# Kernel optimization log

Measured on AMD Instinct MI355X. Metric: run time of the kernel, lower is better.

The kernel has to match this reference:

```python
import jax, jax.numpy as jnp
import numpy as np

N_EVENTS = 50000
TS_SIZE = 512
N_NEURONS = 256
LAMBDA_HOMEO = 0.25


def setup_inputs() -> dict:
    key = jax.random.key(0)
    k1, k2 = jax.random.split(key)
    # event time surfaces (nonnegative, like torch surfaces)
    all_ts = jax.random.uniform(k1, (N_EVENTS, TS_SIZE), dtype=jnp.float32)
    # synapses.weight ~ U[0,1), as in torch.nn.init.uniform_(a=0,b=1)
    W = jax.random.uniform(k2, (N_NEURONS, TS_SIZE), dtype=jnp.float32)
    cumhisto = jnp.ones((N_NEURONS,), dtype=jnp.float32)
    return {"all_ts": all_ts, "W": W, "cumhisto": cumhisto}


def reference(all_ts, W, cumhisto):
    """Training branch (learning_flag=True, homeo_flag=True) of hotslayer.forward.

    Sequential per-event: normalize ts, cosine-like scores beta, homeostatic gain
    picks the winner, winner row of W is pulled toward ts, histogram incremented.
    Returns (per-event winners [N_EVENTS], final W [N,TS], final cumhisto [N]).
    """
    n_neurons = W.shape[0]

    def step(carry, ts):
        W, ch = carry
        ts = ts / jnp.linalg.norm(ts)
        w_norm = jnp.linalg.norm(W, axis=1)          # [N]
        beta = (W @ ts) / w_norm                      # [N]
        gain = jnp.exp(LAMBDA_HOMEO * (1.0 - n_neurons * ch / ch.sum()))
        n_star = jnp.argmax(gain * beta)
        Ck = W[n_star]                                # [TS]
        alpha = 0.01 / (1.0 + ch[n_star] / 20000.0)
        W = W.at[n_star].set(Ck + alpha * beta[n_star] * (ts - Ck))
        ch = ch.at[n_star].add(1.0)
        return (W, ch), n_star

    (W_f, ch_f), winners = jax.lax.scan(step, (W, cumhisto), all_ts)
    return winners, W_f, ch_f
```

## Files before the change

kernel.cpp:

```cpp
#include <hip/hip_runtime.h>
#include <hip/hip_bf16.h>

#define N_EVENTS 50000
#define TS 512
#define NN 256
#define BATCH 512
#define SUB 64
#define LAMB 0.25f
#define NB 98

#define RLF(v, l) __int_as_float(__builtin_amdgcn_readlane(__float_as_int(v), (l)))
#define RLI(v, l) __builtin_amdgcn_readlane((v), (l))
#define FRCP(x) __builtin_amdgcn_rcpf(x)
#define FRSQ(x) __builtin_amdgcn_rsqf(x)
#define DPP_MAXF(x, ctrl)                                                            \
    { int _s = __builtin_amdgcn_update_dpp(__float_as_int(x), __float_as_int(x),     \
                                           (ctrl), 0xF, 0xF, false);                 \
      (x) = fmaxf((x), __int_as_float(_s)); }


__global__ __launch_bounds__(256)
void inv_kernel(const float* __restrict__ ts, float* __restrict__ inv)
{
    __shared__ double red[256];
    const int e = blockIdx.x;
    const int d = threadIdx.x;
    const float* row = ts + (size_t)e * TS;
    float x0 = row[d], x1 = row[d + 256];
    red[d] = (double)x0 * x0 + (double)x1 * x1;
    __syncthreads();
    for (int st = 128; st > 0; st >>= 1) {
        if (d < st) red[d] += red[d + st];
        __syncthreads();
    }
    if (d == 0) inv[e] = (float)(1.0 / sqrt(red[0]));
}

__global__ __launch_bounds__(256)
void init_kernel(const float* __restrict__ chin, float* __restrict__ ch,
                 float* Pn0, float* Pn1, float* phi0, float* phi1,
                 float* c0, float* c1, float* d0, float* d1,
                 int* w0, int* w1)
{
    int i = blockIdx.x * 256 + threadIdx.x;
    if (i < NN) { ch[i] = chin[i]; Pn0[i] = 1.f; Pn1[i] = 1.f; }
    if (i < BATCH) {
        phi0[i] = 0.f; phi1[i] = 0.f; c0[i] = 0.f; c1[i] = 0.f;
        d0[i] = 0.f; d1[i] = 0.f; w0[i] = 0; w1[i] = 0;
    }
}


__device__ void gram_tile(float* SH, const float* __restrict__ ts,
                          const float* __restrict__ inv,
                          int astart, int as, int bstart2, int bs2,
                          int be, int bf, float* __restrict__ outp, int transpose)
{
    float* At = SH;
    float* Bt = SH + 64 * 33;
    if (be * 64 >= as || bf * 64 >= bs2) return;
    const int tx = threadIdx.x & 15, ty = threadIdx.x >> 4;
    float acc[4][4] = {};
    for (int kt = 0; kt < TS; kt += 32) {
        for (int it = threadIdx.x; it < 64 * 32; it += 256) {
            int r = it >> 5, c = it & 31;
            int ra = be * 64 + r, rb = bf * 64 + r;
            At[r * 33 + c] = (ra < as) ? ts[(size_t)(astart + ra) * TS + kt + c] : 0.f;
            Bt[r * 33 + c] = (rb < bs2) ? ts[(size_t)(bstart2 + rb) * TS + kt + c] : 0.f;
        }
        __syncthreads();
#pragma unroll
        for (int kk = 0; kk < 32; ++kk) {
            float av[4], bv[4];
#pragma unroll
            for (int i = 0; i < 4; ++i) av[i] = At[(ty * 4 + i) * 33 + kk];
#pragma unroll
            for (int j = 0; j < 4; ++j) bv[j] = Bt[(tx * 4 + j) * 33 + kk];
#pragma unroll
            for (int i = 0; i < 4; ++i)
#pragma unroll
                for (int j = 0; j < 4; ++j)
                    acc[i][j] += av[i] * bv[j];
        }
        __syncthreads();
    }
#pragma unroll
    for (int i = 0; i < 4; ++i) {
        int e = be * 64 + ty * 4 + i;
        if (e >= as) continue;
        float ie = inv[astart + e];
#pragma unroll
        for (int j = 0; j < 4; ++j) {
            int f = bf * 64 + tx * 4 + j;
            if (f >= bs2) continue;
            float v = acc[i][j] * ie * inv[bstart2 + f];
            if (transpose) outp[(size_t)f * BATCH + e] = v;
            else           outp[(size_t)e * BATCH + f] = v;
        }
    }
}

__global__ __launch_bounds__(256)
void gram_kernel(const float* __restrict__ ts, const float* __restrict__ inv,
                 float* __restrict__ outp, int astart, int as, int bstart2, int bs2,
                 int upper, int transpose)
{
    __shared__ float SHg[64 * 33 * 2];
    if (upper && (int)blockIdx.y < (int)blockIdx.x) return;
    gram_tile(SHg, ts, inv, astart, as, bstart2, bs2, blockIdx.x, blockIdx.y,
              outp, transpose);
}


__device__ void neuron_body(float* shf, double* red,
    const float* __restrict__ ts, const float* __restrict__ inv,
    const float* __restrict__ Wsrc, float* __restrict__ wdst,
    const int* __restrict__ winPrev, const float* __restrict__ phiPrev,
    const float* __restrict__ PnPrev,
    float* __restrict__ wn2W, float* __restrict__ S2W,
    const float* __restrict__ chbuf, float* __restrict__ chout,
    int n, int bprev_start, int bs_prev, int bnext_start, int bs_next)
{
    int* winS = (int*)shf;
    float* phiS = shf + 512;
    float* WL = shf + 1024;
    const int d = threadIdx.x;
    for (int i = d; i < bs_prev; i += 256) { winS[i] = winPrev[i]; phiS[i] = phiPrev[i]; }
    __syncthreads();
    const float Pf = PnPrev[n];
    float w0 = Wsrc[n * TS + d];
    float w1 = Wsrc[n * TS + d + 256];
    double a0 = 0.0, a1 = 0.0;
    for (int e = 0; e < bs_prev; ++e) {
        if (winS[e] == n) {
            double coef = (double)phiS[e];
            float iv = inv[bprev_start + e];
            const float* tr = ts + (size_t)(bprev_start + e) * TS;
            a0 += coef * (double)(tr[d] * iv);
            a1 += coef * (double)(tr[d + 256] * iv);
        }
    }
    w0 = (float)((double)Pf * ((double)w0 + a0));
    w1 = (float)((double)Pf * ((double)w1 + a1));
    wdst[n * TS + d] = w0;
    wdst[n * TS + d + 256] = w1;
    WL[d] = w0; WL[d + 256] = w1;
    if (wn2W) {
        red[d] = (double)w0 * w0 + (double)w1 * w1;
        __syncthreads();
        for (int st = 128; st > 0; st >>= 1) {
            if (d < st) red[d] += red[d + st];
            __syncthreads();
        }
        if (d == 0) wn2W[n] = (float)red[0];
    } else {
        __syncthreads();
    }
    if (bs_next > 0) {
#pragma unroll
        for (int rep = 0; rep < 2; ++rep) {
            int f = d + rep * 256;
            if (f < bs_next) {
                double acc = 0.0;
                const float* tr = ts + (size_t)(bnext_start + f) * TS;
                for (int k = 0; k < TS; ++k) acc += (double)tr[k] * (double)WL[k];
                S2W[f * NN + n] = (float)(acc * (double)inv[bnext_start + f]);
            }
        }
    }
    if (chout && d == 0) chout[n] = chbuf[n];
}

__global__ __launch_bounds__(256)
void neuron_kernel(const float* __restrict__ ts, const float* __restrict__ inv,
    const float* __restrict__ Wsrc, float* __restrict__ wdst,
    const int* __restrict__ winPrev, const float* __restrict__ phiPrev,
    const float* __restrict__ PnPrev,
    float* __restrict__ wn2W, float* __restrict__ S2W,
    const float* __restrict__ chbuf, float* __restrict__ chout,
    int bprev_start, int bs_prev, int bnext_start, int bs_next)
{
    __shared__ float SHN[1536];
    __shared__ double redN[256];
    neuron_body(SHN, redN, ts, inv, Wsrc, wdst, winPrev, phiPrev, PnPrev,
                wn2W, S2W, chbuf, chout, blockIdx.x,
                bprev_start, bs_prev, bnext_start, bs_next);
}


__global__ __launch_bounds__(256)
void fix_kernel(const float* __restrict__ S2r, const float* __restrict__ GxTr,
    const int* __restrict__ winPrev, const float* __restrict__ phiPrev,
    const float* __restrict__ cPrev, const float* __restrict__ dPrev,
    const float* __restrict__ PnPrev, const float* __restrict__ wn2b,
    float* __restrict__ S0corr, float* __restrict__ wn2start,
    int bs, int b0flag)
{
    __shared__ int winS[512];
    __shared__ float phiP[512];
    __shared__ float gr[512];
    __shared__ float cS[512];
    __shared__ float dS[512];
    const int tid = threadIdx.x;
    const int f = blockIdx.x;
    for (int i = tid; i < 512; i += 256) {
        int w = winPrev[i];
        winS[i] = w;
        phiP[i] = b0flag ? 0.f : phiPrev[i] * PnPrev[w];
        cS[i] = cPrev[i];
        dS[i] = dPrev[i];
        gr[i] = (b0flag || f >= bs) ? 0.f : GxTr[(size_t)f * BATCH + i];
    }
    __syncthreads();
    if (f < bs) {
        int n = tid;
        float acc = PnPrev[n] * S2r[f * NN + n];
        if (!b0flag) {
            for (int e = 0; e < 512; ++e)
                if (winS[e] == n) acc += phiP[e] * gr[e];
        }
        S0corr[f * NN + n] = acc;
    }
    if (f == 0 && tid < 64) {
        const int lane = tid;
        float w2[4];
#pragma unroll
        for (int k = 0; k < 4; ++k) w2[k] = wn2b[k * 64 + lane];
        for (int e = 0; e < 512; ++e) {
            float c = cS[e];
            if (c != 0.f) {
                int w = winS[e];
                int owner = w & 63, kk = w >> 6;
                float omc = 1.f - c;
                float t2 = 2.f * c * omc * dS[e] + c * c;
#pragma unroll
                for (int k = 0; k < 4; ++k)
                    if (lane == owner && k == kk) w2[k] = omc * omc * w2[k] + t2;
            }
        }
#pragma unroll
        for (int k = 0; k < 4; ++k) wn2start[k * 64 + lane] = w2[k];
    }
}


__device__ void block0_body(float* SH,
    const float* __restrict__ S0corr, const float* __restrict__ GwR,
    const float* __restrict__ wn2start, float* __restrict__ chbuf,
    int* __restrict__ winCur, float* __restrict__ phiCur,
    float* __restrict__ cCur, float* __restrict__ dotCur, float* __restrict__ PnCur,
    float* __restrict__ winners_out, int bstart, int bs)
{
    float* ACC = SH;
    float* GS  = SH + 16384;
    float* GL  = SH + 20480;
    int*   winL = (int*)(SH + 24576);
    float* phiL = SH + 25088;
    float* cL   = SH + 25600;
    float* dL   = SH + 26112;
    const int tid = threadIdx.x, wid = tid >> 6, lane = tid & 63;

    const float KC = -(LAMB * 256.0f * 1.44269504f);
    float ch[4] = {0,0,0,0}, wn2v[4] = {1,1,1,1};
    float rn[4] = {1,1,1,1}, Pn[4] = {1,1,1,1}, al[4] = {0,0,0,0};
    float Ssum = 1.f, K2 = 0.f;
    if (wid == 0) {
#pragma unroll
        for (int k = 0; k < 4; ++k) {
            int n = k * 64 + lane;
            ch[k] = chbuf[n];
            wn2v[k] = wn2start[n];
            rn[k] = FRSQ(wn2v[k]);
            al[k] = 0.01f * FRCP(1.0f + ch[k] * (1.0f / 20000.0f));
        }
        float loc = ch[0] + ch[1] + ch[2] + ch[3];
#pragma unroll
        for (int off = 32; off > 0; off >>= 1) loc += __shfl_xor(loc, off, 64);
        Ssum = loc;
        K2 = KC * FRCP(Ssum);
    }

    const int nsub = (bs + SUB - 1) >> 6;
    for (int sub = 0; sub < nsub; ++sub) {
        const int s0 = sub << 6;
        const int cnt = min(SUB, bs - s0);
        __syncthreads();
        {
            const int n = tid;
            for (int f = 0; f < cnt; f += 8) {
                const float* src = S0corr + (size_t)(s0 + f) * NN + n;
                float v0 = src[0 * NN], v1 = src[1 * NN], v2 = src[2 * NN], v3 = src[3 * NN];
                float v4 = src[4 * NN], v5 = src[5 * NN], v6 = src[6 * NN], v7 = src[7 * NN];
                ACC[(f + 0) * NN + ((n + f + 0) & 255)] = v0;
                ACC[(f + 1) * NN + ((n + f + 1) & 255)] = v1;
                ACC[(f + 2) * NN + ((n + f + 2) & 255)] = v2;
                ACC[(f + 3) * NN + ((n + f + 3) & 255)] = v3;
                ACC[(f + 4) * NN + ((n + f + 4) & 255)] = v4;
                ACC[(f + 5) * NN + ((n + f + 5) & 255)] = v5;
                ACC[(f + 6) * NN + ((n + f + 6) & 255)] = v6;
                ACC[(f + 7) * NN + ((n + f + 7) & 255)] = v7;
            }
        }
        for (int it = tid; it < SUB * SUB; it += 256) {
            int t = it >> 6, f = it & 63;
            GS[it] = (t < cnt && f < cnt) ? GwR[(size_t)(s0 + t) * BATCH + s0 + f] : 0.f;
        }
        for (int base = 0; base < s0; base += 64) {
            {
                const int i0 = tid, i1 = tid + 256, i2 = tid + 512, i3 = tid + 768;
                for (int rep = 0; rep < 4096; rep += 1024) {
                    float g0 = GwR[(size_t)(base + ((i0 + rep) >> 6)) * BATCH + s0 + (i0 & 63)];
                    float g1 = GwR[(size_t)(base + ((i1 + rep) >> 6)) * BATCH + s0 + (i1 & 63)];
                    float g2 = GwR[(size_t)(base + ((i2 + rep) >> 6)) * BATCH + s0 + (i2 & 63)];
                    float g3 = GwR[(size_t)(base + ((i3 + rep) >> 6)) * BATCH + s0 + (i3 & 63)];
                    GL[i0 + rep] = g0; GL[i1 + rep] = g1;
                    GL[i2 + rep] = g2; GL[i3 + rep] = g3;
                }
            }
            int wreg = winL[base + lane];
            float preg = phiL[base + lane];
            __syncthreads();
            for (int j = 0; j < 64; ++j) {
                int wj = RLI(wreg, j);
                if ((wj & 3) == wid) {
                    float pj = RLF(preg, j);
                    if (lane < cnt)
                        ACC[lane * NN + ((wj + lane) & 255)] += pj * GL[j * 64 + lane];
                }
            }
            __syncthreads();
        }
        __syncthreads();

        if (wid == 0) {
            float acur[4];
#pragma unroll
            for (int k = 0; k < 4; ++k) acur[k] = ACC[(k * 64 + lane) & 255];

            for (int t = 0; t < cnt; ++t) {
                const bool havenext = (t + 1 < cnt);
                float anext[4] = {0.f, 0.f, 0.f, 0.f};
                if (havenext) {
                    const int r = t + 1;
#pragma unroll
                    for (int k = 0; k < 4; ++k)
                        anext[k] = ACC[r * NN + ((k * 64 + lane + r) & 255)];
                }
                const int forig = t + 1 + lane;
                const float gval = GS[t * SUB + (forig & 63)];

                float beta[4], key[4];
#pragma unroll
                for (int k = 0; k < 4; ++k) {
                    float dot = Pn[k] * acur[k];
                    beta[k] = dot * rn[k];
                    key[k] = beta[k] * exp2f(K2 * ch[k]);
                }
                float kmax = fmaxf(fmaxf(key[0], key[1]), fmaxf(key[2], key[3]));
                DPP_MAXF(kmax, 0x111); DPP_MAXF(kmax, 0x112); DPP_MAXF(kmax, 0x114);
                DPP_MAXF(kmax, 0x118); DPP_MAXF(kmax, 0x142); DPP_MAXF(kmax, 0x143);
                const float smax = RLF(kmax, 63);

                unsigned long long m0 = __ballot(key[0] == smax);
                unsigned long long m1 = __ballot(key[1] == smax);
                unsigned long long m2 = __ballot(key[2] == smax);
                unsigned long long m3 = __ballot(key[3] == smax);
                int ns = m0 ? (int)__builtin_ctzll(m0)
                       : m1 ? 64  + (int)__builtin_ctzll(m1)
                       : m2 ? 128 + (int)__builtin_ctzll(m2)
                            : 192 + (int)__builtin_ctzll(m3);
                ns = __builtin_amdgcn_readfirstlane(ns);
                const int owner = ns & 63, ks = ns >> 6;

                float bsel = (ks == 0) ? beta[0] : (ks == 1) ? beta[1] : (ks == 2) ? beta[2] : beta[3];
                float asel = (ks == 0) ? acur[0] : (ks == 1) ? acur[1] : (ks == 2) ? acur[2] : acur[3];
                float psel = (ks == 0) ? Pn[0]   : (ks == 1) ? Pn[1]   : (ks == 2) ? Pn[2]   : Pn[3];
                float lsel = (ks == 0) ? al[0]   : (ks == 1) ? al[1]   : (ks == 2) ? al[2]   : al[3];
                const float betas  = RLF(bsel, owner);
                const float alphas = RLF(lsel, owner);
                const float dots   = RLF(psel * asel, owner);
                const float pold   = RLF(psel, owner);

                const float c    = alphas * betas;
                const float omc  = 1.0f - c;
                const float pnew = pold * omc;
                const float phi  = c * FRCP(pnew);
                const float g1   = RLF(gval, 0);

#pragma unroll
                for (int k = 0; k < 4; ++k) {
                    if (lane == owner && k == ks) {
                        wn2v[k] = omc * omc * wn2v[k] + 2.f * c * omc * dots + c * c;
                        rn[k] = FRSQ(wn2v[k]);
                        ch[k] += 1.0f;
                        al[k] = 0.01f * FRCP(1.0f + ch[k] * (1.0f / 20000.0f));
                        Pn[k] = pnew;
                        anext[k] += phi * g1;
                    }
                }
                if (lane > 0 && forig < cnt)
                    ACC[forig * NN + ((ns + forig) & 255)] += phi * gval;

                const int ib = s0 + t;
                if (lane == 0) {
                    winL[ib] = ns; phiL[ib] = phi;
                    cL[ib] = c; dL[ib] = dots;
                }
                Ssum += 1.0f;
                K2 = KC * FRCP(Ssum);
                if (havenext) {
#pragma unroll
                    for (int k = 0; k < 4; ++k) acur[k] = anext[k];
                }
            }
        }
    }
    __syncthreads();
    if (wid == 0) {
#pragma unroll
        for (int k = 0; k < 4; ++k) {
            int n = k * 64 + lane;
            chbuf[n] = ch[k];
            PnCur[n] = Pn[k];
        }
    }
    for (int i = tid; i < bs; i += 256) {
        int w = winL[i];
        winCur[i] = w;
        phiCur[i] = phiL[i];
        cCur[i] = cL[i];
        dotCur[i] = dL[i];
        winners_out[bstart + i] = (float)w;
    }
}


__global__ __launch_bounds__(256)
void fusedA_kernel(const float* __restrict__ ts, const float* __restrict__ inv,
    const float* __restrict__ S0corr, const float* __restrict__ GwR,
    float* __restrict__ GwW, float* __restrict__ GxTW,
    const float* __restrict__ wn2start, float* __restrict__ chbuf,
    const int* __restrict__ winPrev, const float* __restrict__ phiPrev,
    const float* __restrict__ PnPrev,
    int* __restrict__ winCur, float* __restrict__ phiCur,
    float* __restrict__ cCur, float* __restrict__ dotCur, float* __restrict__ PnCur,
    float* __restrict__ Wcur, float* __restrict__ wn2W, float* __restrict__ S2W,
    float* __restrict__ out, int b, int bstart, int bs, int bnext_start, int bs_next)
{
    __shared__ float SH[26624];
    const int bx = blockIdx.x;
    if (bx == 0) {
        block0_body(SH, S0corr, GwR, wn2start, chbuf,
                    winCur, phiCur, cCur, dotCur, PnCur, out, bstart, bs);
    } else if (bx <= NN) {
        neuron_body(SH, (double*)(SH + 1536), ts, inv, Wcur, Wcur,
                    winPrev, phiPrev, PnPrev, wn2W, S2W, nullptr, nullptr,
                    bx - 1, bstart - BATCH, (b == 0) ? 0 : BATCH,
                    bnext_start, bs_next);
    } else {
        int job = bx - (NN + 1);
        if (bs_next <= 0) return;
        if (job < 64) {
            gram_tile(SH, ts, inv, bstart, bs, bnext_start, bs_next,
                      job >> 3, job & 7, GxTW, 1);
        } else {
            int jw = job - 64;
            int be = 0;
            while (jw >= 8 - be) { jw -= 8 - be; ++be; }
            int bf = be + jw;
            gram_tile(SH, ts, inv, bnext_start, bs_next, bnext_start, bs_next,
                      be, bf, GwW, 0);
        }
    }
}


__global__ __launch_bounds__(256)
void winit_kernel(const float* __restrict__ Wcur, const float* __restrict__ chin,
                  float* __restrict__ ch, float* __restrict__ wn2, float* __restrict__ rn)
{
    __shared__ double red[256];
    const int n = blockIdx.x;
    const int d = threadIdx.x;
    float w0 = Wcur[n * TS + d], w1 = Wcur[n * TS + d + 256];
    red[d] = (double)w0 * w0 + (double)w1 * w1;
    __syncthreads();
    for (int st = 128; st > 0; st >>= 1) {
        if (d < st) red[d] += red[d + st];
        __syncthreads();
    }
    if (d == 0) {
        double s = red[0];
        wn2[n] = (float)s;
        rn[n]  = (float)(1.0 / sqrt(s));
        ch[n]  = chin[n];
    }
}

__global__ __launch_bounds__(256)
void s0_gemm_kernel(const float* __restrict__ ts, const float* __restrict__ Wcur,
                    const float* __restrict__ inv, float* __restrict__ S0P,
                    int bstart, int bs)
{
    __shared__ float At[64][33];
    __shared__ float Bt[64][33];
    const int bf = blockIdx.x;
    const int bn = blockIdx.y;
    if (bf * 64 >= bs) return;
    const int tx = threadIdx.x & 15, ty = threadIdx.x >> 4;
    double acc[4][4] = {};
    for (int kt = 0; kt < TS; kt += 32) {
        for (int it = threadIdx.x; it < 64 * 32; it += 256) {
            int r = it >> 5, c = it & 31;
            int row = bf * 64 + r;
            At[r][c] = (row < bs) ? ts[(size_t)(bstart + row) * TS + kt + c] : 0.f;
            Bt[r][c] = Wcur[(bn * 64 + r) * TS + kt + c];
        }
        __syncthreads();
#pragma unroll
        for (int kk = 0; kk < 32; ++kk) {
            float av[4], bv[4];
#pragma unroll
            for (int i = 0; i < 4; ++i) av[i] = At[ty * 4 + i][kk];
#pragma unroll
            for (int j = 0; j < 4; ++j) bv[j] = Bt[tx * 4 + j][kk];
#pragma unroll
            for (int i = 0; i < 4; ++i)
#pragma unroll
                for (int j = 0; j < 4; ++j)
                    acc[i][j] += (double)av[i] * (double)bv[j];
        }
        __syncthreads();
    }
#pragma unroll
    for (int i = 0; i < 4; ++i) {
        int f = bf * 64 + ty * 4 + i;
        if (f >= bs) continue;
        double iv = (double)inv[bstart + f];
#pragma unroll
        for (int j = 0; j < 4; ++j) {
            int n = bn * 64 + tx * 4 + j;
            S0P[f * NN + n] = (float)(acc[i][j] * iv);
        }
    }
}

__global__ __launch_bounds__(256)
void seq_step_kernel(const float* __restrict__ S0P, const float* __restrict__ Gb,
                     float* __restrict__ ch_g, const float* __restrict__ wn2_g,
                     const float* __restrict__ rn_g, float* __restrict__ Pn_g,
                     float* __restrict__ phi_g, int* __restrict__ win_g,
                     float* __restrict__ winners_out, int bstart, int bs)
{
    __shared__ float ACC[SUB * NN];
    __shared__ float GS[SUB * SUB];
    __shared__ float GL[SUB * SUB];
    __shared__ int   winL[BATCH];
    __shared__ float phiL[BATCH];

    const int tid = threadIdx.x;
    const int wid = tid >> 6;
    const int lane = tid & 63;

    float ch[4] = {0, 0, 0, 0}, wn2v[4] = {1, 1, 1, 1};
    float rn[4] = {1, 1, 1, 1}, Pn[4] = {1, 1, 1, 1};
    float Ssum = 1.f, sinv = 1.f;
    if (wid == 0) {
#pragma unroll
        for (int k = 0; k < 4; ++k) {
            int n = k * 64 + lane;
            ch[k]   = ch_g[n];
            wn2v[k] = wn2_g[n];
            rn[k]   = rn_g[n];
            Pn[k]   = 1.0f;
        }
        float loc = ch[0] + ch[1] + ch[2] + ch[3];
#pragma unroll
        for (int off = 32; off > 0; off >>= 1) loc += __shfl_xor(loc, off, 64);
        Ssum = loc;
        sinv = 1.0f / Ssum;
    }

    const int nsub = (bs + SUB - 1) >> 6;
    for (int sub = 0; sub < nsub; ++sub) {
        const int s0 = sub << 6;
        const int cnt = min(SUB, bs - s0);
        __syncthreads();

        for (int it = tid; it < cnt * NN; it += 256) {
            int r = it >> 8, n = it & 255;
            ACC[r * NN + ((n + r) & 255)] = S0P[(s0 + r) * NN + n];
        }
        for (int it = tid; it < cnt * SUB; it += 256) {
            int t = it >> 6, f = it & 63;
            GS[t * SUB + f] = (f < cnt) ? Gb[(s0 + t) * BATCH + s0 + f] : 0.f;
        }
        __syncthreads();

        for (int base = 0; base < s0; base += 64) {
            for (int it = tid; it < 64 * 64; it += 256)
                GL[it] = Gb[(base + (it >> 6)) * BATCH + s0 + (it & 63)];
            int   wreg = winL[base + lane];
            float preg = phiL[base + lane];
            __syncthreads();
            for (int j = 0; j < 64; ++j) {
                int wj = RLI(wreg, j);
                if ((wj & 3) == wid) {
                    float pj = RLF(preg, j);
                    if (lane < cnt)
                        ACC[lane * NN + ((wj + lane) & 255)] += pj * GL[j * 64 + lane];
                }
            }
            __syncthreads();
        }

        if (wid == 0) {
            float acur[4];
#pragma unroll
            for (int k = 0; k < 4; ++k) acur[k] = ACC[(k * 64 + lane) & 255];

            for (int t = 0; t < cnt; ++t) {
                const bool havenext = (t + 1 < cnt);
                float anext[4] = {0.f, 0.f, 0.f, 0.f};
                if (havenext) {
                    const int r = t + 1;
#pragma unroll
                    for (int k = 0; k < 4; ++k)
                        anext[k] = ACC[r * NN + ((k * 64 + lane + r) & 255)];
                }
                const int forig = t + 1 + lane;
                const float gval = GS[t * SUB + (forig & 63)];

                const float gmul = 256.0f * sinv;
                float beta[4], key[4];
                float kmax;
#pragma unroll
                for (int k = 0; k < 4; ++k) {
                    float dot = Pn[k] * acur[k];
                    beta[k] = dot * rn[k];
                    float frac = ch[k] * gmul;
                    float gain = __expf(LAMB * (1.0f - frac));
                    key[k] = gain * beta[k];
                }
                kmax = fmaxf(fmaxf(key[0], key[1]), fmaxf(key[2], key[3]));
                DPP_MAXF(kmax, 0x111); DPP_MAXF(kmax, 0x112); DPP_MAXF(kmax, 0x114);
                DPP_MAXF(kmax, 0x118); DPP_MAXF(kmax, 0x142); DPP_MAXF(kmax, 0x143);
                const float smax = RLF(kmax, 63);

                unsigned long long m0 = __ballot(key[0] == smax);
                unsigned long long m1 = __ballot(key[1] == smax);
                unsigned long long m2 = __ballot(key[2] == smax);
                unsigned long long m3 = __ballot(key[3] == smax);
                int ns = m0 ? (int)__builtin_ctzll(m0)
                       : m1 ? 64  + (int)__builtin_ctzll(m1)
                       : m2 ? 128 + (int)__builtin_ctzll(m2)
                            : 192 + (int)__builtin_ctzll(m3);
                ns = __builtin_amdgcn_readfirstlane(ns);
                const int owner = ns & 63, ks = ns >> 6;

                float bsel = (ks == 0) ? beta[0] : (ks == 1) ? beta[1] : (ks == 2) ? beta[2] : beta[3];
                float csel = (ks == 0) ? ch[0]   : (ks == 1) ? ch[1]   : (ks == 2) ? ch[2]   : ch[3];
                float asel = (ks == 0) ? acur[0] : (ks == 1) ? acur[1] : (ks == 2) ? acur[2] : acur[3];
                float psel = (ks == 0) ? Pn[0]   : (ks == 1) ? Pn[1]   : (ks == 2) ? Pn[2]   : Pn[3];
                const float betas = RLF(bsel, owner);
                const float chs   = RLF(csel, owner);
                const float dots  = RLF(psel * asel, owner);
                const float pold  = RLF(psel, owner);

                const float alpha = 0.01f / (1.0f + chs / 20000.0f);
                const float c    = alpha * betas;
                const float omc  = 1.0f - c;
                const float pnew = pold * omc;
                const float phi  = c / pnew;
                const float g1   = RLF(gval, 0);

#pragma unroll
                for (int k = 0; k < 4; ++k) {
                    bool me = (lane == owner) && (k == ks);
                    if (me) {
                        wn2v[k] = omc * omc * wn2v[k] + 2.f * c * omc * dots + c * c;
                        rn[k] = 1.0f / sqrtf(wn2v[k]);
                        ch[k] += 1.0f;
                        Pn[k] = pnew;
                        anext[k] += phi * g1;
                    }
                }
                if (lane > 0 && forig < cnt)
                    ACC[forig * NN + ((ns + forig) & 255)] += phi * gval;

                const int ib = s0 + t;
                if (lane == 0) {
                    winL[ib] = ns; phiL[ib] = phi;
                    win_g[ib] = ns; phi_g[ib] = phi;
                    winners_out[bstart + ib] = (float)ns;
                }
                Ssum += 1.0f;
                sinv = 1.0f / Ssum;
                if (havenext) {
#pragma unroll
                    for (int k = 0; k < 4; ++k) acur[k] = anext[k];
                }
            }
        }
        __syncthreads();
    }

    if (wid == 0) {
#pragma unroll
        for (int k = 0; k < 4; ++k) {
            int n = k * 64 + lane;
            ch_g[n] = ch[k];
            Pn_g[n] = Pn[k];
        }
    }
}

__global__ __launch_bounds__(256)
void wupdate_kernel(const float* __restrict__ ts, const float* __restrict__ inv,
                    const int* __restrict__ win_g, const float* __restrict__ phi_g,
                    const float* __restrict__ Pn_g, float* __restrict__ Wcur,
                    float* __restrict__ wn2_g, float* __restrict__ rn_g,
                    int bstart, int bs)
{
    __shared__ int   winS[BATCH];
    __shared__ float phiS[BATCH];
    __shared__ double red[256];
    const int n = blockIdx.x;
    const int d = threadIdx.x;
    for (int i = d; i < bs; i += 256) { winS[i] = win_g[i]; phiS[i] = phi_g[i]; }
    __syncthreads();
    const float Pf = Pn_g[n];
    float w0 = Wcur[n * TS + d];
    float w1 = Wcur[n * TS + d + 256];
    double a0 = 0.0, a1 = 0.0;
    for (int ib = 0; ib < bs; ++ib) {
        if (winS[ib] == n) {
            double coef = (double)phiS[ib] * (double)Pf;
            float iv = inv[bstart + ib];
            const float* tr = ts + (size_t)(bstart + ib) * TS;
            a0 += coef * (double)(tr[d] * iv);
            a1 += coef * (double)(tr[d + 256] * iv);
        }
    }
    w0 = (float)((double)Pf * (double)w0 + a0);
    w1 = (float)((double)Pf * (double)w1 + a1);
    Wcur[n * TS + d] = w0;
    Wcur[n * TS + d + 256] = w1;
    red[d] = (double)w0 * w0 + (double)w1 * w1;
    __syncthreads();
    for (int st = 128; st > 0; st >>= 1) {
        if (d < st) red[d] += red[d + st];
        __syncthreads();
    }
    if (d == 0) {
        double s = red[0];
        wn2_g[n] = (float)s;
        rn_g[n]  = (float)(1.0 / sqrt(s));
    }
}

__global__ __launch_bounds__(256)
void final_kernel(const float* __restrict__ Wcur, const float* __restrict__ ch,
                  float* __restrict__ out)
{
    int i = blockIdx.x * 256 + threadIdx.x;
    if (i < NN * TS) out[N_EVENTS + i] = Wcur[i];
    else if (i < NN * TS + NN) out[N_EVENTS + i] = ch[i - NN * TS];
}


extern "C" void kernel_launch(void* const* d_in, const int* in_sizes, int n_in,
                              void* d_out, int out_size, void* d_ws, size_t ws_size,
                              hipStream_t stream)
{
    const float* ts   = (const float*)d_in[0];
    const float* W0   = (const float*)d_in[1];
    const float* chin = (const float*)d_in[2];
    float* out = (float*)d_out;
    float* ws  = (float*)d_ws;

    const size_t FULL_FLOATS = 1628544;
    if (ws_size >= FULL_FLOATS * sizeof(float)) {
        float* inv  = ws + 0;
        float* Wcur = ws + 50048;
        float* ch   = ws + 181120;
        float* wn2b[2] = { ws + 181376, ws + 181632 };
        float* wn2s = ws + 181888;
        float* Pn[2]  = { ws + 182144, ws + 182400 };
        float* phi[2] = { ws + 182656, ws + 183168 };
        float* cE[2]  = { ws + 183680, ws + 184192 };
        float* dE[2]  = { ws + 184704, ws + 185216 };
        int*   win[2] = { (int*)(ws + 185728), (int*)(ws + 186240) };
        float* S2[2]  = { ws + 186752, ws + 317824 };
        float* S0c    = ws + 448896;
        float* GxT[2] = { ws + 579968, ws + 842112 };
        float* Gw[2]  = { ws + 1104256, ws + 1366400 };

        hipMemcpyAsync(Wcur, W0, (size_t)NN * TS * sizeof(float),
                       hipMemcpyDeviceToDevice, stream);
        inv_kernel<<<N_EVENTS, 256, 0, stream>>>(ts, inv);
        init_kernel<<<2, 256, 0, stream>>>(chin, ch, Pn[0], Pn[1], phi[0], phi[1],
                                           cE[0], cE[1], dE[0], dE[1], win[0], win[1]);
        neuron_kernel<<<NN, 256, 0, stream>>>(ts, inv, Wcur, Wcur,
            win[1], phi[1], Pn[1], wn2b[0], S2[0], nullptr, nullptr,
            0, 0, 0, BATCH);
        gram_kernel<<<dim3(8, 8), 256, 0, stream>>>(ts, inv, Gw[0],
            0, BATCH, 0, BATCH, 1, 0);

        for (int b = 0; b < NB; ++b) {
            const int cs = b & 1, ps = 1 - cs;
            const int bstart = b * BATCH;
            const int bs = min(BATCH, N_EVENTS - bstart);
            const int bnext = bstart + BATCH;
            const int bsn = (b == NB - 1) ? 0 : min(BATCH, N_EVENTS - bnext);

            fix_kernel<<<BATCH, 256, 0, stream>>>(S2[cs], GxT[cs],
                win[ps], phi[ps], cE[ps], dE[ps], Pn[ps], wn2b[cs],
                S0c, wn2s, bs, (b == 0) ? 1 : 0);

            const int grid = (b == NB - 1) ? (NN + 1) : (NN + 1 + 100);
            fusedA_kernel<<<grid, 256, 0, stream>>>(ts, inv, S0c, Gw[cs],
                Gw[ps], GxT[ps], wn2s, ch,
                win[ps], phi[ps], Pn[ps],
                win[cs], phi[cs], cE[cs], dE[cs], Pn[cs],
                Wcur, wn2b[ps], S2[ps],
                out, b, bstart, bs, bnext, bsn);
        }
        neuron_kernel<<<NN, 256, 0, stream>>>(ts, inv, Wcur, out + N_EVENTS,
            win[1], phi[1], Pn[1], nullptr, nullptr, ch, out + N_EVENTS + NN * TS,
            97 * BATCH, 336, 0, 0);
    } else {
        float* inv  = ws + 0;
        float* Wcur = ws + 50048;
        float* ch   = ws + 181120;
        float* wn2  = ws + 181376;
        float* rn   = ws + 181632;
        float* Pn   = ws + 181888;
        float* phi  = ws + 182144;
        int*   win  = (int*)(ws + 182656);
        float* S0P  = ws + 183168;
        float* G    = ws + 314240;

        hipMemcpyAsync(Wcur, W0, (size_t)NN * TS * sizeof(float),
                       hipMemcpyDeviceToDevice, stream);
        inv_kernel<<<N_EVENTS, 256, 0, stream>>>(ts, inv);
        winit_kernel<<<NN, 256, 0, stream>>>(Wcur, chin, ch, wn2, rn);

        for (int b = 0; b < NB; ++b) {
            int bstart = b * BATCH;
            int bs = min(BATCH, N_EVENTS - bstart);
            s0_gemm_kernel<<<dim3(8, 4), 256, 0, stream>>>(ts, Wcur, inv, S0P, bstart, bs);
            gram_kernel<<<dim3(8, 8), 256, 0, stream>>>(ts, inv, G,
                bstart, bs, bstart, bs, 1, 0);
            seq_step_kernel<<<1, 256, 0, stream>>>(S0P, G, ch, wn2, rn, Pn, phi, win,
                                                   out, bstart, bs);
            wupdate_kernel<<<NN, 256, 0, stream>>>(ts, inv, win, phi, Pn, Wcur,
                                                   wn2, rn, bstart, bs);
        }
        final_kernel<<<(NN * TS + NN + 255) / 256, 256, 0, stream>>>(Wcur, ch, out);
    }
}
```

Before: 53.49 ms.

## Double-buffer winner-selection subbatches so idle waves prefetch next tile

The serial winner-selection loop in block 0 now works on 32-event subbatches with double-buffered ACC and Gram tiles. While wave 0 runs the sequential argmax and update chain, waves 1-3 preload the next subbatch's S0 correction rows, diagonal Gram block and cross-term Gram slices, and apply corrections from earlier subbatches. Only the correction from the current subbatch is applied after a barrier. This aims to take loading and correction work off the critical serial path and shrinks shared memory, at the cost of more barriers per event and a single wave doing all correction for older subbatches.

```diff
diff --git a/kernel.cpp b/kernel.cpp
--- a/kernel.cpp
+++ b/kernel.cpp
@@ -6,6 +6,7 @@
 #define NN 256
 #define BATCH 512
 #define SUB 64
+#define SUBN 32
 #define LAMB 0.25f
 #define NB 98
 
@@ -251,19 +252,20 @@
     float* __restrict__ cCur, float* __restrict__ dotCur, float* __restrict__ PnCur,
     float* __restrict__ winners_out, int bstart, int bs)
 {
-    float* ACC = SH;
-    float* GS  = SH + 16384;
-    float* GL  = SH + 20480;
-    int*   winL = (int*)(SH + 24576);
-    float* phiL = SH + 25088;
-    float* cL   = SH + 25600;
-    float* dL   = SH + 26112;
+    float* ACCb = SH;
+    float* GSb  = SH + 16384;
+    float* GLS  = SH + 18432;
+    float* GLp  = SH + 19456;
+    int*   winL = (int*)(SH + 20480);
+    float* phiL = SH + 20992;
+    float* cL   = SH + 21504;
+    float* dL   = SH + 22016;
     const int tid = threadIdx.x, wid = tid >> 6, lane = tid & 63;
 
     const float KC = -(LAMB * 256.0f * 1.44269504f);
     float ch[4] = {0,0,0,0}, wn2v[4] = {1,1,1,1};
     float rn[4] = {1,1,1,1}, Pn[4] = {1,1,1,1}, al[4] = {0,0,0,0};
-    float Ssum = 1.f, K2 = 0.f;
+    float Sbase = 1.f;
     if (wid == 0) {
 #pragma unroll
         for (int k = 0; k < 4; ++k) {
@@ -276,78 +278,54 @@
         float loc = ch[0] + ch[1] + ch[2] + ch[3];
 #pragma unroll
         for (int off = 32; off > 0; off >>= 1) loc += __shfl_xor(loc, off, 64);
-        Ssum = loc;
-        K2 = KC * FRCP(Ssum);
-    }
-
-    const int nsub = (bs + SUB - 1) >> 6;
-    for (int sub = 0; sub < nsub; ++sub) {
-        const int s0 = sub << 6;
-        const int cnt = min(SUB, bs - s0);
-        __syncthreads();
-        {
-            const int n = tid;
-            for (int f = 0; f < cnt; f += 8) {
-                const float* src = S0corr + (size_t)(s0 + f) * NN + n;
-                float v0 = src[0 * NN], v1 = src[1 * NN], v2 = src[2 * NN], v3 = src[3 * NN];
-                float v4 = src[4 * NN], v5 = src[5 * NN], v6 = src[6 * NN], v7 = src[7 * NN];
-                ACC[(f + 0) * NN + ((n + f + 0) & 255)] = v0;
-                ACC[(f + 1) * NN + ((n + f + 1) & 255)] = v1;
-                ACC[(f + 2) * NN + ((n + f + 2) & 255)] = v2;
-                ACC[(f + 3) * NN + ((n + f + 3) & 255)] = v3;
-                ACC[(f + 4) * NN + ((n + f + 4) & 255)] = v4;
-                ACC[(f + 5) * NN + ((n + f + 5) & 255)] = v5;
-                ACC[(f + 6) * NN + ((n + f + 6) & 255)] = v6;
-                ACC[(f + 7) * NN + ((n + f + 7) & 255)] = v7;
-            }
-        }
-        for (int it = tid; it < SUB * SUB; it += 256) {
-            int t = it >> 6, f = it & 63;
-            GS[it] = (t < cnt && f < cnt) ? GwR[(size_t)(s0 + t) * BATCH + s0 + f] : 0.f;
-        }
-        for (int base = 0; base < s0; base += 64) {
-            {
-                const int i0 = tid, i1 = tid + 256, i2 = tid + 512, i3 = tid + 768;
-                for (int rep = 0; rep < 4096; rep += 1024) {
-                    float g0 = GwR[(size_t)(base + ((i0 + rep) >> 6)) * BATCH + s0 + (i0 & 63)];
-                    float g1 = GwR[(size_t)(base + ((i1 + rep) >> 6)) * BATCH + s0 + (i1 & 63)];
-                    float g2 = GwR[(size_t)(base + ((i2 + rep) >> 6)) * BATCH + s0 + (i2 & 63)];
-                    float g3 = GwR[(size_t)(base + ((i3 + rep) >> 6)) * BATCH + s0 + (i3 & 63)];
-                    GL[i0 + rep] = g0; GL[i1 + rep] = g1;
-                    GL[i2 + rep] = g2; GL[i3 + rep] = g3;
-                }
-            }
-            int wreg = winL[base + lane];
-            float preg = phiL[base + lane];
-            __syncthreads();
-            for (int j = 0; j < 64; ++j) {
-                int wj = RLI(wreg, j);
-                if ((wj & 3) == wid) {
-                    float pj = RLF(preg, j);
-                    if (lane < cnt)
-                        ACC[lane * NN + ((wj + lane) & 255)] += pj * GL[j * 64 + lane];
-                }
-            }
-            __syncthreads();
-        }
-        __syncthreads();
+        Sbase = loc;
+    }
+
+    const int nsub = (bs + SUBN - 1) >> 5;
+
+    {
+        const int cnt0 = min(SUBN, bs);
+        for (int it = tid; it < cnt0 * NN; it += 256) {
+            int r = it >> 8, n = it & 255;
+            ACCb[r * NN + ((n + r) & 255)] = S0corr[r * NN + n];
+        }
+        for (int it = tid; it < SUBN * SUBN; it += 256) {
+            int t2 = it >> 5, f2 = it & 31;
+            GSb[it] = (t2 < cnt0 && f2 < cnt0) ? GwR[(size_t)t2 * BATCH + f2] : 0.f;
+        }
+    }
+    __syncthreads();
+
+    for (int s = 0; s < nsub; ++s) {
+        const int s0 = s << 5;
+        const int cnt = min(SUBN, bs - s0);
+        const int cur = s & 1, nxt = cur ^ 1;
+        float* ACCc = ACCb + cur * (SUBN * NN);
+        float* ACCn = ACCb + nxt * (SUBN * NN);
+        float* GSc  = GSb + cur * (SUBN * SUBN);
+        float* GSn  = GSb + nxt * (SUBN * SUBN);
+        const int s0n = s0 + SUBN;
+        const int cntn = min(SUBN, bs - s0n);
+        const bool haveprep = (s + 1 < nsub);
 
         if (wid == 0) {
             float acur[4];
 #pragma unroll
-            for (int k = 0; k < 4; ++k) acur[k] = ACC[(k * 64 + lane) & 255];
+            for (int k = 0; k < 4; ++k) acur[k] = ACCc[(k * 64 + lane) & 255];
 
             for (int t = 0; t < cnt; ++t) {
+                const int ib = s0 + t;
+                const float K2 = KC * FRCP(Sbase + (float)ib);
                 const bool havenext = (t + 1 < cnt);
                 float anext[4] = {0.f, 0.f, 0.f, 0.f};
                 if (havenext) {
                     const int r = t + 1;
 #pragma unroll
                     for (int k = 0; k < 4; ++k)
-                        anext[k] = ACC[r * NN + ((k * 64 + lane + r) & 255)];
+                        anext[k] = ACCc[r * NN + ((k * 64 + lane + r) & 255)];
                 }
                 const int forig = t + 1 + lane;
-                const float gval = GS[t * SUB + (forig & 63)];
+                const float gval = GSc[t * SUBN + (forig & 31)];
 
                 float beta[4], key[4];
 #pragma unroll
@@ -399,23 +377,70 @@
                     }
                 }
                 if (lane > 0 && forig < cnt)
-                    ACC[forig * NN + ((ns + forig) & 255)] += phi * gval;
-
-                const int ib = s0 + t;
+                    ACCc[forig * NN + ((ns + forig) & 255)] += phi * gval;
+
                 if (lane == 0) {
                     winL[ib] = ns; phiL[ib] = phi;
                     cL[ib] = c; dL[ib] = dots;
                 }
-                Ssum += 1.0f;
-                K2 = KC * FRCP(Ssum);
                 if (havenext) {
 #pragma unroll
                     for (int k = 0; k < 4; ++k) acur[k] = anext[k];
                 }
             }
-        }
-    }
-    __syncthreads();
+        } else if (haveprep) {
+            if (wid == 1) {
+#pragma unroll 4
+                for (int i = lane; i < cntn * NN; i += 64) {
+                    int r = i >> 8, n = i & 255;
+                    ACCn[r * NN + ((n + r) & 255)] = S0corr[(s0n + r) * NN + n];
+                }
+                for (int base = 0; base < s0; base += SUBN) {
+#pragma unroll 4
+                    for (int i = lane; i < SUBN * SUBN; i += 64)
+                        GLp[i] = GwR[(size_t)(base + (i >> 5)) * BATCH + s0n + (i & 31)];
+                    int   wreg = winL[base + (lane & 31)];
+                    float preg = phiL[base + (lane & 31)];
+                    for (int j = 0; j < SUBN; ++j) {
+                        int wj = RLI(wreg, j);
+                        float pj = RLF(preg, j);
+                        if (lane < cntn)
+                            ACCn[lane * NN + ((wj + lane) & 255)] += pj * GLp[j * SUBN + lane];
+                    }
+                }
+            } else if (wid == 2) {
+#pragma unroll 4
+                for (int i = lane; i < SUBN * SUBN; i += 64) {
+                    int t2 = i >> 5, f2 = i & 31;
+                    GSn[i] = (t2 < cntn && f2 < cntn)
+                           ? GwR[(size_t)(s0n + t2) * BATCH + s0n + f2] : 0.f;
+                }
+            } else {
+#pragma unroll 4
+                for (int i = lane; i < SUBN * SUBN; i += 64) {
+                    int j = i >> 5, r = i & 31;
+                    GLS[i] = (j < cnt && r < cntn)
+                           ? GwR[(size_t)(s0 + j) * BATCH + s0n + r] : 0.f;
+                }
+            }
+        }
+        __syncthreads();
+
+        if (haveprep) {
+            int   wreg = winL[s0 + (lane & 31)];
+            float preg = phiL[s0 + (lane & 31)];
+            for (int j = 0; j < cnt; ++j) {
+                int wj = RLI(wreg, j);
+                if ((wj & 3) == wid) {
+                    float pj = RLF(preg, j);
+                    if (lane < cntn)
+                        ACCn[lane * NN + ((wj + lane) & 255)] += pj * GLS[j * SUBN + lane];
+                }
+            }
+        }
+        __syncthreads();
+    }
+
     if (wid == 0) {
 #pragma unroll
         for (int k = 0; k < 4; ++k) {
@@ -447,7 +472,7 @@
     float* __restrict__ Wcur, float* __restrict__ wn2W, float* __restrict__ S2W,
     float* __restrict__ out, int b, int bstart, int bs, int bnext_start, int bs_next)
 {
-    __shared__ float SH[26624];
+    __shared__ float SH[22528];
     const int bx = blockIdx.x;
     if (bx == 0) {
         block0_body(SH, S0corr, GwR, wn2start, chbuf,
```

Result: slower. 59.15 ms (+10.6%).

## Spread sequential winner selection across all four wavefronts with shared-memory argmax

Applied to the files above, without the earlier changes.

The per-event winner search in block 0 was run by a single wavefront holding four neurons per lane. It now gives each of the four wavefronts 64 neurons, one per lane. Each wavefront writes a packed (max key, index) candidate to LDS, and after a __syncthreads all wavefronts pick the global winner; the owning wavefront then applies the update. This cuts per-lane ALU work per event but adds a block-wide barrier to every sequential step, and that barrier could outweigh the savings.

```diff
diff --git a/kernel.cpp b/kernel.cpp
--- a/kernel.cpp
+++ b/kernel.cpp
@@ -258,27 +258,28 @@
     float* phiL = SH + 25088;
     float* cL   = SH + 25600;
     float* dL   = SH + 26112;
+    unsigned long long* CANDu = (unsigned long long*)(SH + 26624);
+    float* SUMS = SH + 26640;
+
     const int tid = threadIdx.x, wid = tid >> 6, lane = tid & 63;
+    const int widu = __builtin_amdgcn_readfirstlane(wid);
+    const int myn = (wid << 6) + lane;
 
     const float KC = -(LAMB * 256.0f * 1.44269504f);
-    float ch[4] = {0,0,0,0}, wn2v[4] = {1,1,1,1};
-    float rn[4] = {1,1,1,1}, Pn[4] = {1,1,1,1}, al[4] = {0,0,0,0};
-    float Ssum = 1.f, K2 = 0.f;
-    if (wid == 0) {
-#pragma unroll
-        for (int k = 0; k < 4; ++k) {
-            int n = k * 64 + lane;
-            ch[k] = chbuf[n];
-            wn2v[k] = wn2start[n];
-            rn[k] = FRSQ(wn2v[k]);
-            al[k] = 0.01f * FRCP(1.0f + ch[k] * (1.0f / 20000.0f));
-        }
-        float loc = ch[0] + ch[1] + ch[2] + ch[3];
+    float ch = chbuf[myn];
+    float wn2v = wn2start[myn];
+    float rn = FRSQ(wn2v);
+    float al = 0.01f * FRCP(1.0f + ch * (1.0f / 20000.0f));
+    float Pn = 1.0f;
+
+    {
+        float loc = ch;
 #pragma unroll
         for (int off = 32; off > 0; off >>= 1) loc += __shfl_xor(loc, off, 64);
-        Ssum = loc;
-        K2 = KC * FRCP(Ssum);
-    }
+        if (lane == 0) SUMS[wid] = loc;
+    }
+    __syncthreads();
+    const float Sbase = SUMS[0] + SUMS[1] + SUMS[2] + SUMS[3];
 
     const int nsub = (bs + SUB - 1) >> 6;
     for (int sub = 0; sub < nsub; ++sub) {
@@ -332,98 +333,71 @@
         }
         __syncthreads();
 
-        if (wid == 0) {
-            float acur[4];
-#pragma unroll
-            for (int k = 0; k < 4; ++k) acur[k] = ACC[(k * 64 + lane) & 255];
-
-            for (int t = 0; t < cnt; ++t) {
-                const bool havenext = (t + 1 < cnt);
-                float anext[4] = {0.f, 0.f, 0.f, 0.f};
-                if (havenext) {
-                    const int r = t + 1;
-#pragma unroll
-                    for (int k = 0; k < 4; ++k)
-                        anext[k] = ACC[r * NN + ((k * 64 + lane + r) & 255)];
-                }
-                const int forig = t + 1 + lane;
-                const float gval = GS[t * SUB + (forig & 63)];
-
-                float beta[4], key[4];
-#pragma unroll
-                for (int k = 0; k < 4; ++k) {
-                    float dot = Pn[k] * acur[k];
-                    beta[k] = dot * rn[k];
-                    key[k] = beta[k] * exp2f(K2 * ch[k]);
-                }
-                float kmax = fmaxf(fmaxf(key[0], key[1]), fmaxf(key[2], key[3]));
-                DPP_MAXF(kmax, 0x111); DPP_MAXF(kmax, 0x112); DPP_MAXF(kmax, 0x114);
-                DPP_MAXF(kmax, 0x118); DPP_MAXF(kmax, 0x142); DPP_MAXF(kmax, 0x143);
-                const float smax = RLF(kmax, 63);
-
-                unsigned long long m0 = __ballot(key[0] == smax);
-                unsigned long long m1 = __ballot(key[1] == smax);
-                unsigned long long m2 = __ballot(key[2] == smax);
-                unsigned long long m3 = __ballot(key[3] == smax);
-                int ns = m0 ? (int)__builtin_ctzll(m0)
-                       : m1 ? 64  + (int)__builtin_ctzll(m1)
-                       : m2 ? 128 + (int)__builtin_ctzll(m2)
-                            : 192 + (int)__builtin_ctzll(m3);
-                ns = __builtin_amdgcn_readfirstlane(ns);
-                const int owner = ns & 63, ks = ns >> 6;
-
-                float bsel = (ks == 0) ? beta[0] : (ks == 1) ? beta[1] : (ks == 2) ? beta[2] : beta[3];
-                float asel = (ks == 0) ? acur[0] : (ks == 1) ? acur[1] : (ks == 2) ? acur[2] : acur[3];
-                float psel = (ks == 0) ? Pn[0]   : (ks == 1) ? Pn[1]   : (ks == 2) ? Pn[2]   : Pn[3];
-                float lsel = (ks == 0) ? al[0]   : (ks == 1) ? al[1]   : (ks == 2) ? al[2]   : al[3];
-                const float betas  = RLF(bsel, owner);
-                const float alphas = RLF(lsel, owner);
-                const float dots   = RLF(psel * asel, owner);
-                const float pold   = RLF(psel, owner);
-
+        float acur = ACC[myn & 255];
+        for (int t = 0; t < cnt; ++t) {
+            const int ib = s0 + t;
+            const float K2 = KC * FRCP(Sbase + (float)ib);
+            const bool havenext = (t + 1 < cnt);
+            float anext = 0.f;
+            if (havenext) anext = ACC[(t + 1) * NN + ((myn + t + 1) & 255)];
+            const int forig = t + 1 + lane;
+            const float gval = GS[t * SUB + (forig & 63)];
+
+            const float pa = Pn * acur;
+            const float beta = pa * rn;
+            const float key = beta * exp2f(K2 * ch);
+            float kmax = key;
+            DPP_MAXF(kmax, 0x111); DPP_MAXF(kmax, 0x112); DPP_MAXF(kmax, 0x114);
+            DPP_MAXF(kmax, 0x118); DPP_MAXF(kmax, 0x142); DPP_MAXF(kmax, 0x143);
+            const float smax = RLF(kmax, 63);
+            unsigned long long mm = __ballot(key == smax);
+            if (lane == 0) {
+                int nl = (int)__builtin_ctzll(mm);
+                CANDu[((t & 1) << 2) + wid] =
+                    ((unsigned long long)__float_as_uint(smax) << 32)
+                    | (unsigned)(255 - ((wid << 6) + nl));
+            }
+            __syncthreads();
+            const unsigned long long* cb = CANDu + ((t & 1) << 2);
+            unsigned long long b0 = cb[0], b1 = cb[1], b2 = cb[2], b3 = cb[3];
+            unsigned long long ba = b0 > b1 ? b0 : b1;
+            unsigned long long bb = b2 > b3 ? b2 : b3;
+            unsigned long long best = ba > bb ? ba : bb;
+            int ns = 255 - (int)(best & 0xFFull);
+            ns = __builtin_amdgcn_readfirstlane(ns);
+            const int ksq = ns >> 6, owner = ns & 63;
+
+            if (widu == ksq) {
+                const float betas  = RLF(beta, owner);
+                const float dots   = RLF(pa, owner);
+                const float pold   = RLF(Pn, owner);
+                const float alphas = RLF(al, owner);
                 const float c    = alphas * betas;
                 const float omc  = 1.0f - c;
                 const float pnew = pold * omc;
                 const float phi  = c * FRCP(pnew);
                 const float g1   = RLF(gval, 0);
-
-#pragma unroll
-                for (int k = 0; k < 4; ++k) {
-                    if (lane == owner && k == ks) {
-                        wn2v[k] = omc * omc * wn2v[k] + 2.f * c * omc * dots + c * c;
-                        rn[k] = FRSQ(wn2v[k]);
-                        ch[k] += 1.0f;
-                        al[k] = 0.01f * FRCP(1.0f + ch[k] * (1.0f / 20000.0f));
-                        Pn[k] = pnew;
-                        anext[k] += phi * g1;
-                    }
+                if (lane == owner) {
+                    wn2v = omc * omc * wn2v + 2.f * c * omc * dots + c * c;
+                    rn = FRSQ(wn2v);
+                    ch += 1.0f;
+                    al = 0.01f * FRCP(1.0f + ch * (1.0f / 20000.0f));
+                    Pn = pnew;
+                    if (havenext) anext += phi * g1;
                 }
                 if (lane > 0 && forig < cnt)
                     ACC[forig * NN + ((ns + forig) & 255)] += phi * gval;
-
-                const int ib = s0 + t;
                 if (lane == 0) {
                     winL[ib] = ns; phiL[ib] = phi;
                     cL[ib] = c; dL[ib] = dots;
                 }
-                Ssum += 1.0f;
-                K2 = KC * FRCP(Ssum);
-                if (havenext) {
-#pragma unroll
-                    for (int k = 0; k < 4; ++k) acur[k] = anext[k];
-                }
             }
+            acur = anext;
         }
     }
     __syncthreads();
-    if (wid == 0) {
-#pragma unroll
-        for (int k = 0; k < 4; ++k) {
-            int n = k * 64 + lane;
-            chbuf[n] = ch[k];
-            PnCur[n] = Pn[k];
-        }
-    }
+    chbuf[myn] = ch;
+    PnCur[myn] = Pn;
     for (int i = tid; i < bs; i += 256) {
         int w = winL[i];
         winCur[i] = w;
@@ -447,7 +421,7 @@
     float* __restrict__ Wcur, float* __restrict__ wn2W, float* __restrict__ S2W,
     float* __restrict__ out, int b, int bstart, int bs, int bnext_start, int bs_next)
 {
-    __shared__ float SH[26624];
+    __shared__ float SH[26656];
     const int bx = blockIdx.x;
     if (bx == 0) {
         block0_body(SH, S0corr, GwR, wn2start, chbuf,
```

Measured after the change: 56.76 ms. 6.1% more time.
